# Kernel tuning notes

Measured on AMD Instinct MI355X. Metric: run time of the kernel, lower is better.

Reference implementation:

```python
import jax, jax.numpy as jnp
import numpy as np

BATCH = 65536
IN = 256
NCLS = 10
DIMS = [IN, 128, 256, 512, 256, 128, 64, 32, 16, NCLS]
KEEP = 0.7  # dropout p=0.3


def setup_inputs() -> dict:
    key = jax.random.key(0)
    ks = jax.random.split(key, 40)
    d = {"x": jax.random.normal(ks[0], (BATCH, IN), dtype=jnp.float32)}
    # 9 linear layers
    for i in range(9):
        fan_in = DIMS[i]
        d[f"W{i+1}"] = jax.random.normal(ks[1 + 2 * i], (DIMS[i], DIMS[i + 1]), dtype=jnp.float32) / np.sqrt(fan_in)
        d[f"b{i+1}"] = jax.random.normal(ks[2 + 2 * i], (DIMS[i + 1],), dtype=jnp.float32) * 0.01
    # precomputed inverted-dropout masks for the 8 hidden layers (training mode, p=0.3)
    for i in range(8):
        bern = jax.random.bernoulli(ks[20 + i], KEEP, (BATCH, DIMS[i + 1]))
        d[f"m{i+1}"] = bern.astype(jnp.float32) / KEEP
    return d


def reference(x, W1, b1, W2, b2, W3, b3, W4, b4, W5, b5, W6, b6, W7, b7, W8, b8, W9, b9,
              m1, m2, m3, m4, m5, m6, m7, m8):
    Ws = [W1, W2, W3, W4, W5, W6, W7, W8]
    bs = [b1, b2, b3, b4, b5, b6, b7, b8]
    ms = [m1, m2, m3, m4, m5, m6, m7, m8]
    h = x
    for W, b, m in zip(Ws, bs, ms):
        h = jax.nn.relu(h @ W + b) * m  # Linear -> ReLU -> Dropout (inverted mask)
    return h @ W9 + b9
```

## Files before the change

### kernel.cpp

```cpp
#include <hip/hip_runtime.h>
#include <hip/hip_bf16.h>
#include <stdint.h>

typedef __bf16 bf16x8 __attribute__((ext_vector_type(8)));
typedef uint16_t u16x8 __attribute__((ext_vector_type(8)));
typedef float f32x16 __attribute__((ext_vector_type(16)));

static constexpr int KD[9]    = {256,128,256,512,256,128,64,32,16};
static constexpr int ND[9]    = {128,256,512,256,128,64,32,16,10};
static constexpr int NPD[9]   = {128,256,512,256,128,64,32,32,32};
static constexpr int WOFF[10] = {0,32768,65536,196608,327680,360448,368640,370688,371712,372224};
static constexpr int BOFF[10] = {0,128,384,896,1152,1280,1344,1376,1408,1440};
static constexpr int WTOT = 372224;
static constexpr int BTOT = 1440;

__device__ __forceinline__ uint16_t f2bf(float f) {
  uint32_t u = __builtin_bit_cast(uint32_t, f);
  return (uint16_t)((u + 0x7fffu + ((u >> 16) & 1u)) >> 16);
}

constexpr int swzm(int width) {
  return (width >= 128) ? 15 : (width == 64) ? 7 : (width == 32) ? 3 : 1;
}

struct PrepArgs {
  const float* W[9];
  const float* b[9];
  uint16_t* wt;
  float* bias;
};

__global__ void prep_kernel(PrepArgs a) {
  int idx = blockIdx.x * 256 + threadIdx.x;
  if (idx < WTOT) {
#pragma unroll
    for (int l = 0; l < 9; ++l) {
      if (idx >= WOFF[l] && idx < WOFF[l + 1]) {
        const int K = KD[l], N = ND[l], KS = KD[l] / 16;
        int local = idx - WOFF[l];
        int j    = local & 7;
        int g    = local >> 3;
        int lane = g & 63;
        int gg   = g >> 6;
        int ks   = gg % KS;
        int ct   = gg / KS;
        int n = ct * 32 + (lane & 31);
        int k = ks * 16 + (lane >> 5) * 8 + j;
        float v = (n < N) ? a.W[l][(size_t)k * N + n] : 0.0f;
        a.wt[idx] = f2bf(v);
      }
    }
  } else if (idx < WTOT + BTOT) {
    int bidx = idx - WTOT;
#pragma unroll
    for (int l = 0; l < 9; ++l) {
      if (bidx >= BOFF[l] && bidx < BOFF[l + 1]) {
        int n = bidx - BOFF[l];
        a.bias[bidx] = (n < ND[l]) ? a.b[l][n] : 0.0f;
      }
    }
  }
}

struct MainArgs {
  const float* x;
  const float* m[8];
  const uint16_t* wt;
  const float* bias;
  float* out;
};

template <int L, int TNE, int CTOFF, bool LAST, bool SIN, bool PREBAR, int OSTR>
__device__ __forceinline__ void layer_fn(const MainArgs& a, int row0, int wid, int lane,
                                         const char* in0, const char* in1, char* outb) {
  constexpr int K   = KD[L];
  constexpr int N   = ND[L];
  constexpr int KS  = K / 16;
  constexpr int NB  = (TNE >= 4) ? TNE / 4 : 1;
  constexpr int ACT = (TNE >= 4) ? 4 : TNE;
  constexpr int SWZI = swzm(K);
  constexpr int SWZO = swzm(OSTR);
  constexpr bool DUAL = (NB == 1 && KS >= 2);

  const int r  = lane & 31;
  const int kg = lane >> 5;
  const int ct0 = wid * NB;
  const bool act = (wid < ACT);

  f32x16 acc[NB];
  f32x16 acc2;
  float mv[NB][16];
  float bvv[NB];

  if (act) {
#pragma unroll
    for (int i = 0; i < NB; ++i)
#pragma unroll
      for (int t = 0; t < 16; ++t) acc[i][t] = 0.0f;
    if constexpr (DUAL) {
#pragma unroll
      for (int t = 0; t < 16; ++t) acc2[t] = 0.0f;
    }

    const uint16_t* wbase = a.wt + WOFF[L]
        + ((size_t)(CTOFF + ct0) * KS * 64 + lane) * 8;

    bf16x8 bb[2][NB];
#pragma unroll
    for (int i = 0; i < NB; ++i)
      bb[0][i] = *(const bf16x8*)(wbase + (size_t)i * KS * 512);

#pragma unroll
    for (int i = 0; i < NB; ++i) {
      const int col = (CTOFF + ct0 + i) * 32 + r;
      bvv[i] = a.bias[BOFF[L] + col];
      if constexpr (!LAST) {
        const int mc = (N % 32) ? (col < N ? col : N - 1) : col;
        const float* mrow = a.m[L] + mc;
#pragma unroll
        for (int t = 0; t < 16; ++t) {
          const int rit = (t & 3) + ((t >> 2) << 3) + (kg << 2);
          mv[i][t] = mrow[(size_t)(row0 + rit) * N];
        }
      }
    }

#pragma unroll
    for (int ks = 0; ks < KS; ++ks) {
      if (ks + 1 < KS) {
#pragma unroll
        for (int i = 0; i < NB; ++i)
          bb[(ks + 1) & 1][i] =
              *(const bf16x8*)(wbase + (size_t)i * KS * 512 + (size_t)(ks + 1) * 512);
      }
      bf16x8 av;
      {
        uint32_t byte;
        const char* src;
        if constexpr (SIN) {
          const int kk = (ks < 16) ? ks : ks - 16;
          src = (ks < 16) ? in0 : in1;
          byte = (uint32_t)(r * 256 + kk * 16 + kg * 8) * 2;
          byte ^= (uint32_t)(r & 15) << 4;
        } else {
          src = in0;
          byte = (uint32_t)(r * K + ks * 16 + kg * 8) * 2;
          byte ^= (uint32_t)(r & SWZI) << 4;
        }
        av = *(const bf16x8*)(src + byte);
      }
      if constexpr (DUAL) {
        if ((ks & 1) == 0)
          acc[0] = __builtin_amdgcn_mfma_f32_32x32x16_bf16(av, bb[ks & 1][0], acc[0], 0, 0, 0);
        else
          acc2 = __builtin_amdgcn_mfma_f32_32x32x16_bf16(av, bb[ks & 1][0], acc2, 0, 0, 0);
      } else {
#pragma unroll
        for (int i = 0; i < NB; ++i)
          acc[i] = __builtin_amdgcn_mfma_f32_32x32x16_bf16(av, bb[ks & 1][i], acc[i], 0, 0, 0);
      }
    }
    if constexpr (DUAL) acc[0] += acc2;
  }

  if constexpr (PREBAR) __syncthreads();

  if (act) {
#pragma unroll
    for (int i = 0; i < NB; ++i) {
      const int col = (CTOFF + ct0 + i) * 32 + r;
#pragma unroll
      for (int t = 0; t < 16; ++t) {
        const int rit = (t & 3) + ((t >> 2) << 3) + (kg << 2);
        float v = acc[i][t] + bvv[i];
        if constexpr (LAST) {
          if (col < N) a.out[(size_t)(row0 + rit) * N + col] = v;
        } else {
          v = fmaxf(v, 0.0f) * mv[i][t];
          if ((N % 32 == 0) || col < N) {
            uint32_t ob = (uint32_t)(rit * OSTR + (col - CTOFF * 32)) * 2;
            ob ^= (uint32_t)(rit & SWZO) << 4;
            *(uint16_t*)(outb + ob) = f2bf(v);
          }
        }
      }
    }
  }
}

__global__ __launch_bounds__(256, 4) void mlp_kernel(MainArgs a) {
  __shared__ char bufA[16384];
  __shared__ char bufB[16384];

  const int tid = threadIdx.x;
  const int row0 = blockIdx.x * 32;

  {
    const float* xp = a.x + (size_t)row0 * 256;
#pragma unroll
    for (int j = 0; j < 4; ++j) {
      const int cidx = j * 256 + tid;
      const int rr = cidx >> 5;
      const int cc = (cidx & 31) << 3;
      const float4 f0 = *(const float4*)(xp + cidx * 8);
      const float4 f1 = *(const float4*)(xp + cidx * 8 + 4);
      u16x8 h;
      h[0] = f2bf(f0.x); h[1] = f2bf(f0.y); h[2] = f2bf(f0.z); h[3] = f2bf(f0.w);
      h[4] = f2bf(f1.x); h[5] = f2bf(f1.y); h[6] = f2bf(f1.z); h[7] = f2bf(f1.w);
      uint32_t byte = (uint32_t)(rr * 512 + cc * 2) ^ ((uint32_t)(rr & 15) << 4);
      *(u16x8*)(bufA + byte) = h;
    }
  }
  __syncthreads();

  const int lane = tid & 63;
  const int wid = tid >> 6;

  layer_fn<0, 4, 0, false, false, false, 128>(a, row0, wid, lane, bufA, nullptr, bufB); __syncthreads();
  layer_fn<1, 8, 0, false, false, false, 256>(a, row0, wid, lane, bufB, nullptr, bufA); __syncthreads();
  layer_fn<2, 8, 8, false, false, false, 256>(a, row0, wid, lane, bufA, nullptr, bufB);
  layer_fn<2, 8, 0, false, false, true,  256>(a, row0, wid, lane, bufA, nullptr, bufA); __syncthreads();
  layer_fn<3, 8, 0, false, true,  true,  256>(a, row0, wid, lane, bufA, bufB, bufA); __syncthreads();
  layer_fn<4, 4, 0, false, false, false, 128>(a, row0, wid, lane, bufA, nullptr, bufB); __syncthreads();
  layer_fn<5, 2, 0, false, false, false, 64 >(a, row0, wid, lane, bufB, nullptr, bufA); __syncthreads();
  layer_fn<6, 1, 0, false, false, false, 32 >(a, row0, wid, lane, bufA, nullptr, bufB);
  layer_fn<7, 1, 0, false, false, false, 16 >(a, row0, wid, lane, bufB, nullptr, bufA);
  layer_fn<8, 1, 0, true,  false, false, 16 >(a, row0, wid, lane, bufA, nullptr, nullptr);
}

extern "C" void kernel_launch(void* const* d_in, const int* in_sizes, int n_in,
                              void* d_out, int out_size, void* d_ws, size_t ws_size,
                              hipStream_t stream) {
  (void)in_sizes; (void)n_in; (void)out_size; (void)ws_size;

  PrepArgs pa;
  for (int l = 0; l < 9; ++l) {
    pa.W[l] = (const float*)d_in[1 + 2 * l];
    pa.b[l] = (const float*)d_in[2 + 2 * l];
  }
  uint16_t* wt = (uint16_t*)d_ws;
  float* bias = (float*)((char*)d_ws + (size_t)WTOT * 2);
  pa.wt = wt;
  pa.bias = bias;
  prep_kernel<<<dim3((WTOT + BTOT + 255) / 256), dim3(256), 0, stream>>>(pa);

  MainArgs ma;
  ma.x = (const float*)d_in[0];
  for (int i = 0; i < 8; ++i) ma.m[i] = (const float*)d_in[19 + i];
  ma.wt = wt;
  ma.bias = bias;
  ma.out = (float*)d_out;
  mlp_kernel<<<dim3(65536 / 32), dim3(256), 0, stream>>>(ma);
}
```

Before: 143.3 us.

## Prefetch next layer's dropout masks and bias during current layer's MFMA loop

Moves the dropout-mask and bias loads for each layer into the preceding layer's K loop through a prefetch callback, using double-buffered register arrays, so global mask latency overlaps with matrix work. Weight prefetch depth goes from 2 to a 4-slot ring with up to 3 loads in flight. Occupancy in the launch bounds drops from 4 to 3 blocks per CU to make room for the extra registers. This hides memory latency at the cost of higher register pressure and fewer resident waves.

```diff
diff --git a/kernel.cpp b/kernel.cpp
--- a/kernel.cpp
+++ b/kernel.cpp
@@ -8,7 +8,6 @@
 
 static constexpr int KD[9]    = {256,128,256,512,256,128,64,32,16};
 static constexpr int ND[9]    = {128,256,512,256,128,64,32,16,10};
-static constexpr int NPD[9]   = {128,256,512,256,128,64,32,32,32};
 static constexpr int WOFF[10] = {0,32768,65536,196608,327680,360448,368640,370688,371712,372224};
 static constexpr int BOFF[10] = {0,128,384,896,1152,1280,1344,1376,1408,1440};
 static constexpr int WTOT = 372224;
@@ -70,9 +69,37 @@
   float* out;
 };
 
-template <int L, int TNE, int CTOFF, bool LAST, bool SIN, bool PREBAR, int OSTR>
+
+template <int L, int TNE, int CTOFF>
+__device__ __forceinline__ void mask_pf(const MainArgs& a, int row0, int wid, int lane,
+                                        float (&mv)[2][16], float (&bv)[2]) {
+  constexpr int N   = ND[L];
+  constexpr int NB  = (TNE >= 4) ? TNE / 4 : 1;
+  constexpr int ACT = (TNE >= 4) ? 4 : TNE;
+  if (wid >= ACT) return;
+  const int r  = lane & 31;
+  const int kg = lane >> 5;
+#pragma unroll
+  for (int i = 0; i < NB; ++i) {
+    const int col = (CTOFF + wid * NB + i) * 32 + r;
+    bv[i] = a.bias[BOFF[L] + col];
+    if constexpr (L < 8) {
+      const int mc = (N % 32) ? (col < N ? col : N - 1) : col;
+      const float* mrow = a.m[L] + mc;
+#pragma unroll
+      for (int t = 0; t < 16; ++t) {
+        const int rit = (t & 3) + ((t >> 2) << 3) + (kg << 2);
+        mv[i][t] = mrow[(size_t)(row0 + rit) * N];
+      }
+    }
+  }
+}
+
+template <int L, int TNE, int CTOFF, bool LAST, bool SIN, bool PREBAR, int OSTR, typename PF>
 __device__ __forceinline__ void layer_fn(const MainArgs& a, int row0, int wid, int lane,
-                                         const char* in0, const char* in1, char* outb) {
+                                         const char* in0, const char* in1, char* outb,
+                                         const float (&mv)[2][16], const float (&bv)[2],
+                                         PF&& pf) {
   constexpr int K   = KD[L];
   constexpr int N   = ND[L];
   constexpr int KS  = K / 16;
@@ -81,6 +108,8 @@
   constexpr int SWZI = swzm(K);
   constexpr int SWZO = swzm(OSTR);
   constexpr bool DUAL = (NB == 1 && KS >= 2);
+  constexpr int D   = 4;
+  constexpr int PRE = (KS < D - 1) ? KS : D - 1;
 
   const int r  = lane & 31;
   const int kg = lane >> 5;
@@ -89,8 +118,6 @@
 
   f32x16 acc[NB];
   f32x16 acc2;
-  float mv[NB][16];
-  float bvv[NB];
 
   if (act) {
 #pragma unroll
@@ -105,33 +132,21 @@
     const uint16_t* wbase = a.wt + WOFF[L]
         + ((size_t)(CTOFF + ct0) * KS * 64 + lane) * 8;
 
-    bf16x8 bb[2][NB];
-#pragma unroll
-    for (int i = 0; i < NB; ++i)
-      bb[0][i] = *(const bf16x8*)(wbase + (size_t)i * KS * 512);
-
-#pragma unroll
-    for (int i = 0; i < NB; ++i) {
-      const int col = (CTOFF + ct0 + i) * 32 + r;
-      bvv[i] = a.bias[BOFF[L] + col];
-      if constexpr (!LAST) {
-        const int mc = (N % 32) ? (col < N ? col : N - 1) : col;
-        const float* mrow = a.m[L] + mc;
-#pragma unroll
-        for (int t = 0; t < 16; ++t) {
-          const int rit = (t & 3) + ((t >> 2) << 3) + (kg << 2);
-          mv[i][t] = mrow[(size_t)(row0 + rit) * N];
-        }
-      }
-    }
+    bf16x8 bb[D][NB];
+#pragma unroll
+    for (int j = 0; j < PRE; ++j)
+#pragma unroll
+      for (int i = 0; i < NB; ++i)
+        bb[j][i] = *(const bf16x8*)(wbase + (size_t)i * KS * 512 + (size_t)j * 512);
 
 #pragma unroll
     for (int ks = 0; ks < KS; ++ks) {
-      if (ks + 1 < KS) {
+      if (ks == KS - PRE) pf();
+      if (ks + PRE < KS) {
 #pragma unroll
         for (int i = 0; i < NB; ++i)
-          bb[(ks + 1) & 1][i] =
-              *(const bf16x8*)(wbase + (size_t)i * KS * 512 + (size_t)(ks + 1) * 512);
+          bb[(ks + PRE) % D][i] =
+              *(const bf16x8*)(wbase + (size_t)i * KS * 512 + (size_t)(ks + PRE) * 512);
       }
       bf16x8 av;
       {
@@ -151,13 +166,13 @@
       }
       if constexpr (DUAL) {
         if ((ks & 1) == 0)
-          acc[0] = __builtin_amdgcn_mfma_f32_32x32x16_bf16(av, bb[ks & 1][0], acc[0], 0, 0, 0);
+          acc[0] = __builtin_amdgcn_mfma_f32_32x32x16_bf16(av, bb[ks % D][0], acc[0], 0, 0, 0);
         else
-          acc2 = __builtin_amdgcn_mfma_f32_32x32x16_bf16(av, bb[ks & 1][0], acc2, 0, 0, 0);
+          acc2 = __builtin_amdgcn_mfma_f32_32x32x16_bf16(av, bb[ks % D][0], acc2, 0, 0, 0);
       } else {
 #pragma unroll
         for (int i = 0; i < NB; ++i)
-          acc[i] = __builtin_amdgcn_mfma_f32_32x32x16_bf16(av, bb[ks & 1][i], acc[i], 0, 0, 0);
+          acc[i] = __builtin_amdgcn_mfma_f32_32x32x16_bf16(av, bb[ks % D][i], acc[i], 0, 0, 0);
       }
     }
     if constexpr (DUAL) acc[0] += acc2;
@@ -172,7 +187,7 @@
 #pragma unroll
       for (int t = 0; t < 16; ++t) {
         const int rit = (t & 3) + ((t >> 2) << 3) + (kg << 2);
-        float v = acc[i][t] + bvv[i];
+        float v = acc[i][t] + bv[i];
         if constexpr (LAST) {
           if (col < N) a.out[(size_t)(row0 + rit) * N + col] = v;
         } else {
@@ -188,12 +203,19 @@
   }
 }
 
-__global__ __launch_bounds__(256, 4) void mlp_kernel(MainArgs a) {
+__global__ __launch_bounds__(256, 3) void mlp_kernel(MainArgs a) {
   __shared__ char bufA[16384];
   __shared__ char bufB[16384];
 
   const int tid = threadIdx.x;
   const int row0 = blockIdx.x * 32;
+  const int lane = tid & 63;
+  const int wid = tid >> 6;
+
+  float mv0[2][16], mv1[2][16];
+  float bv0[2], bv1[2];
+
+  mask_pf<0, 4, 0>(a, row0, wid, lane, mv0, bv0);
 
   {
     const float* xp = a.x + (size_t)row0 * 256;
@@ -213,19 +235,32 @@
   }
   __syncthreads();
 
-  const int lane = tid & 63;
-  const int wid = tid >> 6;
-
-  layer_fn<0, 4, 0, false, false, false, 128>(a, row0, wid, lane, bufA, nullptr, bufB); __syncthreads();
-  layer_fn<1, 8, 0, false, false, false, 256>(a, row0, wid, lane, bufB, nullptr, bufA); __syncthreads();
-  layer_fn<2, 8, 8, false, false, false, 256>(a, row0, wid, lane, bufA, nullptr, bufB);
-  layer_fn<2, 8, 0, false, false, true,  256>(a, row0, wid, lane, bufA, nullptr, bufA); __syncthreads();
-  layer_fn<3, 8, 0, false, true,  true,  256>(a, row0, wid, lane, bufA, bufB, bufA); __syncthreads();
-  layer_fn<4, 4, 0, false, false, false, 128>(a, row0, wid, lane, bufA, nullptr, bufB); __syncthreads();
-  layer_fn<5, 2, 0, false, false, false, 64 >(a, row0, wid, lane, bufB, nullptr, bufA); __syncthreads();
-  layer_fn<6, 1, 0, false, false, false, 32 >(a, row0, wid, lane, bufA, nullptr, bufB);
-  layer_fn<7, 1, 0, false, false, false, 16 >(a, row0, wid, lane, bufB, nullptr, bufA);
-  layer_fn<8, 1, 0, true,  false, false, 16 >(a, row0, wid, lane, bufA, nullptr, nullptr);
+  layer_fn<0, 4, 0, false, false, false, 128>(a, row0, wid, lane, bufA, nullptr, bufB, mv0, bv0,
+      [&]() { mask_pf<1, 8, 0>(a, row0, wid, lane, mv1, bv1); });
+  __syncthreads();
+  layer_fn<1, 8, 0, false, false, false, 256>(a, row0, wid, lane, bufB, nullptr, bufA, mv1, bv1,
+      [&]() { mask_pf<2, 8, 8>(a, row0, wid, lane, mv0, bv0); });
+  __syncthreads();
+  layer_fn<2, 8, 8, false, false, false, 256>(a, row0, wid, lane, bufA, nullptr, bufB, mv0, bv0,
+      [&]() { mask_pf<2, 8, 0>(a, row0, wid, lane, mv1, bv1); });
+  layer_fn<2, 8, 0, false, false, true,  256>(a, row0, wid, lane, bufA, nullptr, bufA, mv1, bv1,
+      [&]() { mask_pf<3, 8, 0>(a, row0, wid, lane, mv0, bv0); });
+  __syncthreads();
+  layer_fn<3, 8, 0, false, true,  true,  256>(a, row0, wid, lane, bufA, bufB, bufA, mv0, bv0,
+      [&]() { mask_pf<4, 4, 0>(a, row0, wid, lane, mv1, bv1); });
+  __syncthreads();
+  layer_fn<4, 4, 0, false, false, false, 128>(a, row0, wid, lane, bufA, nullptr, bufB, mv1, bv1,
+      [&]() { mask_pf<5, 2, 0>(a, row0, wid, lane, mv0, bv0); });
+  __syncthreads();
+  layer_fn<5, 2, 0, false, false, false, 64 >(a, row0, wid, lane, bufB, nullptr, bufA, mv0, bv0,
+      [&]() { mask_pf<6, 1, 0>(a, row0, wid, lane, mv1, bv1); });
+  __syncthreads();
+  layer_fn<6, 1, 0, false, false, false, 32 >(a, row0, wid, lane, bufA, nullptr, bufB, mv1, bv1,
+      [&]() { mask_pf<7, 1, 0>(a, row0, wid, lane, mv0, bv0); });
+  layer_fn<7, 1, 0, false, false, false, 16 >(a, row0, wid, lane, bufB, nullptr, bufA, mv0, bv0,
+      [&]() { mask_pf<8, 1, 0>(a, row0, wid, lane, mv1, bv1); });
+  layer_fn<8, 1, 0, true,  false, false, 16 >(a, row0, wid, lane, bufA, nullptr, nullptr, mv1, bv1,
+      [&]() {});
 }
 
 extern "C" void kernel_launch(void* const* d_in, const int* in_sizes, int n_in,
```

Result: slower. 174.4 us (+21.7%).
